# Kernel optimization log

Hardware: AMD Instinct MI355X
Metric: run time of the kernel (lower is better)

Reference implementation:

```python
import jax, jax.numpy as jnp
import numpy as np

SCALE = 0.2  # init_kwargs: scale
EPS = 1e-12  # F.normalize default eps


def setup_inputs() -> dict:
    key = jax.random.key(0)
    x = jax.random.normal(key, (8, 2048, 512), dtype=jnp.float32)
    return {"x": x}


def reference(x):
    # x: [B, N, D]
    # F.normalize(x, dim=2): x / max(||x||_2, eps)
    norm = jnp.linalg.norm(x, axis=2, keepdims=True)
    x_norm = x / jnp.maximum(norm, EPS)
    # sim: [B, N, N] = x_norm @ x_norm^T, softmax over last dim
    sim = jnp.einsum('bnd,bmd->bnm', x_norm, x_norm)
    attn = jax.nn.softmax(sim, axis=2)
    # (1 + scale) * x - scale * attn @ x
    out = (1.0 + SCALE) * x - SCALE * jnp.einsum('bnm,bmd->bnd', attn, x)
    return out
```

## Files before the change

kernel.cpp:

```cpp
#include <hip/hip_runtime.h>
#include <stdint.h>

typedef unsigned short ushort_t;
typedef float f32x2 __attribute__((ext_vector_type(2)));
typedef float f32x4 __attribute__((ext_vector_type(4)));
typedef float f32x16 __attribute__((ext_vector_type(16)));
typedef short bf16x8 __attribute__((ext_vector_type(8)));
typedef unsigned short us8 __attribute__((ext_vector_type(8)));

#define BATCH 8
#define SEQ   2048
#define DIM   512
#define KBLK  64
#define NIT   (SEQ / KBLK)
#define LDS_TOTAL 156160

__device__ __forceinline__ ushort_t f2bf(float f) {
  union { float f; uint32_t u; } c; c.f = f;
  uint32_t u = c.u;
  return (ushort_t)((u + 0x7FFFu + ((u >> 16) & 1u)) >> 16);
}
__device__ __forceinline__ uint32_t packbf(float a, float b) {
  return (uint32_t)f2bf(a) | ((uint32_t)f2bf(b) << 16);
}
__device__ __forceinline__ void gload_lds16(const void* g, void* l) {
  __builtin_amdgcn_global_load_lds(
      (const __attribute__((address_space(1))) unsigned int*)g,
      (__attribute__((address_space(3))) unsigned int*)l, 16, 0, 0);
}
#define WAIT_LGKM_BAR() { asm volatile("s_waitcnt lgkmcnt(0)" ::: "memory"); \
  __builtin_amdgcn_s_barrier(); __builtin_amdgcn_sched_barrier(0); }
#define WAIT_ALL_BAR()  { asm volatile("s_waitcnt vmcnt(0) lgkmcnt(0)" ::: "memory"); \
  __builtin_amdgcn_s_barrier(); __builtin_amdgcn_sched_barrier(0); }

__global__ void k_prep(const float* __restrict__ x, ushort_t* __restrict__ xn,
                       ushort_t* __restrict__ vt) {
  __shared__ __align__(16) ushort_t tile[64][512];
  const int tid = threadIdx.x, lane = tid & 63, w = tid >> 6;
  const int b = blockIdx.x >> 5, nt = blockIdx.x & 31;
  const size_t row0 = (size_t)b * SEQ + (size_t)nt * 64;

  for (int j = 0; j < 16; ++j) {
    const int r = w * 16 + j;
    const float* xr = x + (row0 + r) * DIM;
    const float4 a  = ((const float4*)xr)[lane * 2];
    const float4 bb = ((const float4*)xr)[lane * 2 + 1];
    float ss = a.x*a.x + a.y*a.y + a.z*a.z + a.w*a.w
             + bb.x*bb.x + bb.y*bb.y + bb.z*bb.z + bb.w*bb.w;
#pragma unroll
    for (int m = 32; m >= 1; m >>= 1) ss += __shfl_xor(ss, m, 64);
    const float rn = 1.2011224087864498f / sqrtf(fmaxf(ss, 1e-24f));
    us8 nrm, raw;
    nrm[0]=f2bf(a.x*rn);  nrm[1]=f2bf(a.y*rn);  nrm[2]=f2bf(a.z*rn);  nrm[3]=f2bf(a.w*rn);
    nrm[4]=f2bf(bb.x*rn); nrm[5]=f2bf(bb.y*rn); nrm[6]=f2bf(bb.z*rn); nrm[7]=f2bf(bb.w*rn);
    raw[0]=f2bf(a.x);  raw[1]=f2bf(a.y);  raw[2]=f2bf(a.z);  raw[3]=f2bf(a.w);
    raw[4]=f2bf(bb.x); raw[5]=f2bf(bb.y); raw[6]=f2bf(bb.z); raw[7]=f2bf(bb.w);
    *(us8*)(xn + (row0 + r) * DIM + lane * 8) = nrm;
    *(us8*)(&tile[r][lane * 8]) = raw;
  }
  __syncthreads();
#pragma unroll
  for (int pass = 0; pass < 2; ++pass) {
    const int d = pass * 256 + tid;
    ushort_t* dst = vt + ((size_t)b * DIM + d) * SEQ + (size_t)nt * 64;
#pragma unroll
    for (int g = 0; g < 8; ++g) {
      us8 v;
#pragma unroll
      for (int e = 0; e < 8; ++e) v[e] = tile[g * 8 + e][d];
      *(us8*)(dst + g * 8) = v;
    }
  }
}

__launch_bounds__(512, 2)
__global__ void k_attn(const ushort_t* __restrict__ xn, const ushort_t* __restrict__ vt,
                       const float* __restrict__ x, float* __restrict__ out) {
  extern __shared__ char smem[];
  char* const Kb0 = smem;
  char* const Kb1 = smem + 65536;
  ushort_t* const P = (ushort_t*)(smem + 131072);
  float* const Sp   = (float*)(smem + 139264);
  float* const lsum = (float*)(smem + 155648);

  const int tid = threadIdx.x;
  const int lane = tid & 63, w = tid >> 6;
  const int kw = w & 1, qw = (w >> 1) & 1, kd = w >> 2;
  const int l31 = lane & 31, l5 = lane >> 5, l7 = lane & 7;
  const int b = blockIdx.x & 7, qt0 = blockIdx.x >> 3;
  const int q0 = qt0 * 64;

  const ushort_t* xnb = xn + (size_t)b * SEQ * DIM;
  const ushort_t* vtb = vt + (size_t)b * DIM * SEQ;

  bf16x8 qreg[16];
#pragma unroll
  for (int ks = 0; ks < 16; ++ks)
    qreg[ks] = *(const bf16x8*)(xnb + (size_t)(q0 + qw * 32 + l31) * DIM
                                + kd * 256 + ks * 16 + l5 * 8);

  f32x16 acc[2][2] = {};
  float plsum = 0.f;

#pragma unroll
  for (int i = 0; i < 8; ++i) {
    const int row = w * 8 + i;
    gload_lds16(xnb + (size_t)row * DIM + ((lane ^ i) << 3), Kb0 + row * 1024);
  }
  asm volatile("s_waitcnt vmcnt(0)" ::: "memory");
  __builtin_amdgcn_s_barrier();
  __builtin_amdgcn_sched_barrier(0);

  for (int t = 0; t < NIT; ++t) {
    const int k0 = t * KBLK;
    char* const Kc = (t & 1) ? Kb1 : Kb0;
    char* const Kn = (t & 1) ? Kb0 : Kb1;

    f32x16 accS = {};
    const int arow = kw * 32 + l31;
#pragma unroll
    for (int ks = 0; ks < 16; ++ks) {
      const int c = kd * 32 + ks * 2 + l5;
      bf16x8 af = *(const bf16x8*)(Kc + arow * 1024 + ((c ^ l7) << 4));
      accS = __builtin_amdgcn_mfma_f32_32x32x16_bf16(af, qreg[ks], accS, 0, 0, 0);
    }

    if (kd) {
      float* tile = Sp + (kw * 2 + qw) * 1024 + l31 * 32;
#pragma unroll
      for (int j = 0; j < 8; ++j) {
        const int u = (j & 1) + 4 * (j >> 1) + 2 * l5;
        f32x2 v = { accS[2 * j], accS[2 * j + 1] };
        *(f32x2*)(tile + ((u ^ l7) << 1)) = v;
      }
    }
    WAIT_LGKM_BAR();

    bf16x8 vv[2][4];
#pragma unroll
    for (int dt = 0; dt < 2; ++dt)
#pragma unroll
      for (int ks = 0; ks < 4; ++ks)
        vv[dt][ks] = *(const bf16x8*)(vtb + (size_t)(w * 64 + dt * 32 + l31) * SEQ
                                      + k0 + ks * 16 + l5 * 8);

    if (!kd) {
      const float* tile = Sp + (kw * 2 + qw) * 1024 + l31 * 32;
      uint32_t* prow = (uint32_t*)(P + (qw * 32 + l31) * 64);
#pragma unroll
      for (int j = 0; j < 8; ++j) {
        const int u = (j & 1) + 4 * (j >> 1) + 2 * l5;
        f32x2 o = *(const f32x2*)(tile + ((u ^ l7) << 1));
        float p0 = __builtin_amdgcn_exp2f(accS[2 * j]     + o[0]);
        float p1 = __builtin_amdgcn_exp2f(accS[2 * j + 1] + o[1]);
        plsum += p0 + p1;
        const int chunk = (kw * 4 + (j >> 1)) ^ l7;
        prow[chunk * 4 + (j & 1) + 2 * l5] = packbf(p0, p1);
      }
    } else if (t + 1 < NIT) {
      const int sid = w - 4;
#pragma unroll
      for (int i = 0; i < 16; ++i) {
        const int row = sid * 16 + i;
        gload_lds16(xnb + (size_t)(k0 + KBLK + row) * DIM + ((lane ^ (i & 7)) << 3),
                    Kn + row * 1024);
      }
    }
    WAIT_LGKM_BAR();

#pragma unroll
    for (int qt = 0; qt < 2; ++qt) {
#pragma unroll
      for (int ks = 0; ks < 4; ++ks) {
        const int c = (ks * 2 + l5) ^ l7;
        bf16x8 pa = *(const bf16x8*)(P + (qt * 32 + l31) * 64 + c * 8);
        acc[qt][0] = __builtin_amdgcn_mfma_f32_32x32x16_bf16(pa, vv[0][ks], acc[qt][0], 0, 0, 0);
        acc[qt][1] = __builtin_amdgcn_mfma_f32_32x32x16_bf16(pa, vv[1][ks], acc[qt][1], 0, 0, 0);
      }
    }
    WAIT_ALL_BAR();
  }

  if (!kd) {
    plsum += __shfl_xor(plsum, 32, 64);
    if (lane < 32) lsum[kw * 64 + qw * 32 + lane] = plsum;
  }
  float* obuf = (float*)smem;
#pragma unroll
  for (int qt = 0; qt < 2; ++qt)
#pragma unroll
    for (int dt = 0; dt < 2; ++dt) {
      const int d = w * 64 + dt * 32 + l31;
#pragma unroll
      for (int r = 0; r < 16; ++r) {
        const int q = qt * 32 + (r & 3) + 8 * (r >> 2) + 4 * l5;
        const int c = (d >> 2) ^ (q & 7);
        obuf[q * 512 + c * 4 + (d & 3)] = acc[qt][dt][r];
      }
    }
  WAIT_LGKM_BAR();

  const int q = tid >> 3, seg = tid & 7;
  const float s = 0.2f / (lsum[q] + lsum[64 + q]);
  const size_t grow = ((size_t)b * SEQ + q0 + q) * DIM;
#pragma unroll
  for (int i = 0; i < 16; ++i) {
    const int c = seg * 16 + i;
    const int cs = c ^ (q & 7);
    f32x4 a = *(const f32x4*)(obuf + q * 512 + cs * 4);
    const float4 xv = *(const float4*)(x + grow + c * 4);
    float4 o;
    o.x = 1.2f * xv.x - s * a[0];
    o.y = 1.2f * xv.y - s * a[1];
    o.z = 1.2f * xv.z - s * a[2];
    o.w = 1.2f * xv.w - s * a[3];
    *(float4*)(out + grow + c * 4) = o;
  }
}

extern "C" void kernel_launch(void* const* d_in, const int* in_sizes, int n_in,
                              void* d_out, int out_size, void* d_ws, size_t ws_size,
                              hipStream_t stream) {
  const float* x = (const float*)d_in[0];
  float* out = (float*)d_out;
  ushort_t* xn = (ushort_t*)d_ws;
  ushort_t* vt = (ushort_t*)((char*)d_ws + (size_t)BATCH * SEQ * DIM * 2);

  k_prep<<<BATCH * (SEQ / 64), 256, 0, stream>>>(x, xn, vt);
  (void)hipFuncSetAttribute((const void*)k_attn,
                            hipFuncAttributeMaxDynamicSharedMemorySize, LDS_TOTAL);
  k_attn<<<BATCH * SEQ / 64, 512, LDS_TOTAL, stream>>>(xn, vt, x, out);
}
```

Baseline: 226.4 us.

## Rewrite attention with warp-specialized QK/PV waves and fragment-major K/V layouts

Replaces both kernels. The prep kernel now writes normalized K and raw V in MFMA-fragment-major tiled layouts. In the attention kernel, Q is staged once in LDS, and four waves compute QK^T while loading the next K fragments straight into registers. The other four waves do the exp, the P write and the PV MFMAs one step behind, using double-buffered P. This aims to overlap the two matmul phases across waves, remove the LDS double buffer for K, and reduce LDS use. The cost is a serialized two-barrier handoff per tile, heavy register pressure, and an uncoalesced scalar output epilogue.

```diff
diff --git a/kernel.cpp b/kernel.cpp
--- a/kernel.cpp
+++ b/kernel.cpp
@@ -11,211 +11,250 @@
 #define BATCH 8
 #define SEQ   2048
 #define DIM   512
-#define KBLK  64
-#define NIT   (SEQ / KBLK)
-#define LDS_TOTAL 156160
+#define NIT   32
 
 __device__ __forceinline__ ushort_t f2bf(float f) {
   union { float f; uint32_t u; } c; c.f = f;
-  uint32_t u = c.u;
-  return (ushort_t)((u + 0x7FFFu + ((u >> 16) & 1u)) >> 16);
-}
-__device__ __forceinline__ uint32_t packbf(float a, float b) {
-  return (uint32_t)f2bf(a) | ((uint32_t)f2bf(b) << 16);
-}
-__device__ __forceinline__ void gload_lds16(const void* g, void* l) {
-  __builtin_amdgcn_global_load_lds(
-      (const __attribute__((address_space(1))) unsigned int*)g,
-      (__attribute__((address_space(3))) unsigned int*)l, 16, 0, 0);
-}
-#define WAIT_LGKM_BAR() { asm volatile("s_waitcnt lgkmcnt(0)" ::: "memory"); \
-  __builtin_amdgcn_s_barrier(); __builtin_amdgcn_sched_barrier(0); }
-#define WAIT_ALL_BAR()  { asm volatile("s_waitcnt vmcnt(0) lgkmcnt(0)" ::: "memory"); \
-  __builtin_amdgcn_s_barrier(); __builtin_amdgcn_sched_barrier(0); }
-
-__global__ void k_prep(const float* __restrict__ x, ushort_t* __restrict__ xn,
-                       ushort_t* __restrict__ vt) {
-  __shared__ __align__(16) ushort_t tile[64][512];
+  return (ushort_t)((c.u + 0x7FFFu + ((c.u >> 16) & 1u)) >> 16);
+}
+
+__global__ __launch_bounds__(256) void k_prep(const float* __restrict__ x,
+                                              ushort_t* __restrict__ kg,
+                                              ushort_t* __restrict__ vg) {
+  __shared__ ushort_t ln[32 * 512];
+  __shared__ ushort_t rw[32 * 512];
   const int tid = threadIdx.x, lane = tid & 63, w = tid >> 6;
-  const int b = blockIdx.x >> 5, nt = blockIdx.x & 31;
-  const size_t row0 = (size_t)b * SEQ + (size_t)nt * 64;
-
-  for (int j = 0; j < 16; ++j) {
-    const int r = w * 16 + j;
-    const float* xr = x + (row0 + r) * DIM;
-    const float4 a  = ((const float4*)xr)[lane * 2];
-    const float4 bb = ((const float4*)xr)[lane * 2 + 1];
+  const int bs = blockIdx.x;
+  const int b = bs >> 6, sib = bs & 63;
+  const float* xs = x + (size_t)bs * 32 * DIM;
+  ushort_t* kgs = kg + (size_t)bs * 32 * DIM;
+  ushort_t* vgb = vg + (size_t)b * SEQ * DIM;
+
+#pragma unroll
+  for (int j = 0; j < 8; ++j) {
+    const int rl = w * 8 + j;
+    const float4 a = *(const float4*)(xs + (size_t)rl * DIM + lane * 8);
+    const float4 c = *(const float4*)(xs + (size_t)rl * DIM + lane * 8 + 4);
     float ss = a.x*a.x + a.y*a.y + a.z*a.z + a.w*a.w
-             + bb.x*bb.x + bb.y*bb.y + bb.z*bb.z + bb.w*bb.w;
+             + c.x*c.x + c.y*c.y + c.z*c.z + c.w*c.w;
 #pragma unroll
     for (int m = 32; m >= 1; m >>= 1) ss += __shfl_xor(ss, m, 64);
     const float rn = 1.2011224087864498f / sqrtf(fmaxf(ss, 1e-24f));
-    us8 nrm, raw;
-    nrm[0]=f2bf(a.x*rn);  nrm[1]=f2bf(a.y*rn);  nrm[2]=f2bf(a.z*rn);  nrm[3]=f2bf(a.w*rn);
-    nrm[4]=f2bf(bb.x*rn); nrm[5]=f2bf(bb.y*rn); nrm[6]=f2bf(bb.z*rn); nrm[7]=f2bf(bb.w*rn);
-    raw[0]=f2bf(a.x);  raw[1]=f2bf(a.y);  raw[2]=f2bf(a.z);  raw[3]=f2bf(a.w);
-    raw[4]=f2bf(bb.x); raw[5]=f2bf(bb.y); raw[6]=f2bf(bb.z); raw[7]=f2bf(bb.w);
-    *(us8*)(xn + (row0 + r) * DIM + lane * 8) = nrm;
-    *(us8*)(&tile[r][lane * 8]) = raw;
+    us8 nv, rv;
+    nv[0]=f2bf(a.x*rn); nv[1]=f2bf(a.y*rn); nv[2]=f2bf(a.z*rn); nv[3]=f2bf(a.w*rn);
+    nv[4]=f2bf(c.x*rn); nv[5]=f2bf(c.y*rn); nv[6]=f2bf(c.z*rn); nv[7]=f2bf(c.w*rn);
+    rv[0]=f2bf(a.x); rv[1]=f2bf(a.y); rv[2]=f2bf(a.z); rv[3]=f2bf(a.w);
+    rv[4]=f2bf(c.x); rv[5]=f2bf(c.y); rv[6]=f2bf(c.z); rv[7]=f2bf(c.w);
+    *(us8*)(&ln[rl * 512 + ((lane ^ rl) << 3)]) = nv;
+    *(us8*)(&rw[rl * 512 + ((lane ^ rl) << 3)]) = rv;
   }
   __syncthreads();
-#pragma unroll
-  for (int pass = 0; pass < 2; ++pass) {
-    const int d = pass * 256 + tid;
-    ushort_t* dst = vt + ((size_t)b * DIM + d) * SEQ + (size_t)nt * 64;
-#pragma unroll
-    for (int g = 0; g < 8; ++g) {
-      us8 v;
-#pragma unroll
-      for (int e = 0; e < 8; ++e) v[e] = tile[g * 8 + e][d];
-      *(us8*)(dst + g * 8) = v;
-    }
-  }
-}
-
-__launch_bounds__(512, 2)
-__global__ void k_attn(const ushort_t* __restrict__ xn, const ushort_t* __restrict__ vt,
-                       const float* __restrict__ x, float* __restrict__ out) {
+
+  const int k32 = tid & 31, g = tid >> 5;
+#pragma unroll
+  for (int p = 0; p < 4; ++p) {
+    const int ks = p * 8 + g;
+    const us8 e0 = *(const us8*)(&ln[k32 * 512 + (((2 * ks)     ^ k32) << 3)]);
+    const us8 e1 = *(const us8*)(&ln[k32 * 512 + (((2 * ks + 1) ^ k32) << 3)]);
+    *(us8*)(kgs + ks * 512 + k32 * 16)     = e0;
+    *(us8*)(kgs + ks * 512 + k32 * 16 + 8) = e1;
+  }
+#pragma unroll
+  for (int p = 0; p < 4; ++p) {
+    const int blk = p * 8 + g;
+    const int kh = blk >> 4, db = blk & 15;
+    const int cch = db * 4 + (k32 >> 3);
+    us8 v0, v1;
+#pragma unroll
+    for (int j = 0; j < 8; ++j) {
+      const int ka = kh * 16 + j;
+      const int kb = kh * 16 + 8 + j;
+      v0[j] = rw[ka * 512 + ((cch ^ ka) << 3) + (k32 & 7)];
+      v1[j] = rw[kb * 512 + ((cch ^ kb) << 3) + (k32 & 7)];
+    }
+    ushort_t* dst = vgb + ((size_t)(sib * 2 + kh) * 16 + db) * 512 + k32 * 16;
+    *(us8*)(dst)     = v0;
+    *(us8*)(dst + 8) = v1;
+  }
+}
+
+#define LSP   65536
+#define LP0   98304
+#define LP1   106496
+#define LRED  114688
+#define LDS_TOTAL 115712
+
+__global__ __launch_bounds__(512, 2) void k_attn(const ushort_t* __restrict__ kg,
+                                                 const ushort_t* __restrict__ vg,
+                                                 const float* __restrict__ x,
+                                                 float* __restrict__ out) {
   extern __shared__ char smem[];
-  char* const Kb0 = smem;
-  char* const Kb1 = smem + 65536;
-  ushort_t* const P = (ushort_t*)(smem + 131072);
-  float* const Sp   = (float*)(smem + 139264);
-  float* const lsum = (float*)(smem + 155648);
-
-  const int tid = threadIdx.x;
-  const int lane = tid & 63, w = tid >> 6;
-  const int kw = w & 1, qw = (w >> 1) & 1, kd = w >> 2;
-  const int l31 = lane & 31, l5 = lane >> 5, l7 = lane & 7;
+  ushort_t* const Qs = (ushort_t*)smem;
+  float* const Sp = (float*)(smem + LSP);
+  float* const lred = (float*)(smem + LRED);
+
+  const int tid = threadIdx.x, lane = tid & 63, w = tid >> 6;
+  const int l31 = lane & 31, l5 = lane >> 5;
   const int b = blockIdx.x & 7, qt0 = blockIdx.x >> 3;
-  const int q0 = qt0 * 64;
-
-  const ushort_t* xnb = xn + (size_t)b * SEQ * DIM;
-  const ushort_t* vtb = vt + (size_t)b * DIM * SEQ;
-
-  bf16x8 qreg[16];
-#pragma unroll
-  for (int ks = 0; ks < 16; ++ks)
-    qreg[ks] = *(const bf16x8*)(xnb + (size_t)(q0 + qw * 32 + l31) * DIM
-                                + kd * 256 + ks * 16 + l5 * 8);
-
-  f32x16 acc[2][2] = {};
+  const ushort_t* kgb = kg + (size_t)b * SEQ * DIM;
+  const ushort_t* vgb = vg + (size_t)b * SEQ * DIM;
+
+  {
+    const int r = tid >> 3;
+    const size_t strip = (size_t)(qt0 * 2 + (r >> 5));
+#pragma unroll
+    for (int it = 0; it < 8; ++it) {
+      const int s = it * 8 + (tid & 7);
+      const int c = s ^ (r & 31);
+      const bf16x8 v = *(const bf16x8*)(kgb + strip * 16384
+                          + (c >> 1) * 512 + (r & 31) * 16 + (c & 1) * 8);
+      *(bf16x8*)(Qs + r * 512 + s * 8) = v;
+    }
+  }
+  const bool isQK = (w < 4);
+  const int kw = w & 1, kd = (w >> 1) & 1;
+  const int jv = w - 4;
+
+  bf16x8 acur[16];
+  bf16x8 vcur[16];
+  f32x16 acc[2][4];
   float plsum = 0.f;
 
-#pragma unroll
-  for (int i = 0; i < 8; ++i) {
-    const int row = w * 8 + i;
-    gload_lds16(xnb + (size_t)row * DIM + ((lane ^ i) << 3), Kb0 + row * 1024);
-  }
-  asm volatile("s_waitcnt vmcnt(0)" ::: "memory");
+  if (isQK) {
+#pragma unroll
+    for (int ks = 0; ks < 16; ++ks)
+      acur[ks] = *(const bf16x8*)(kgb + (size_t)kw * 16384
+                    + (kd * 16 + ks) * 512 + l31 * 16 + l5 * 8);
+  } else {
+    const f32x16 z = {};
+#pragma unroll
+    for (int qt = 0; qt < 2; ++qt)
+#pragma unroll
+      for (int dt = 0; dt < 4; ++dt) acc[qt][dt] = z;
+  }
+  asm volatile("s_waitcnt lgkmcnt(0)" ::: "memory");
   __builtin_amdgcn_s_barrier();
   __builtin_amdgcn_sched_barrier(0);
 
   for (int t = 0; t < NIT; ++t) {
-    const int k0 = t * KBLK;
-    char* const Kc = (t & 1) ? Kb1 : Kb0;
-    char* const Kn = (t & 1) ? Kb0 : Kb1;
-
-    f32x16 accS = {};
-    const int arow = kw * 32 + l31;
-#pragma unroll
-    for (int ks = 0; ks < 16; ++ks) {
-      const int c = kd * 32 + ks * 2 + l5;
-      bf16x8 af = *(const bf16x8*)(Kc + arow * 1024 + ((c ^ l7) << 4));
-      accS = __builtin_amdgcn_mfma_f32_32x32x16_bf16(af, qreg[ks], accS, 0, 0, 0);
-    }
-
-    if (kd) {
-      float* tile = Sp + (kw * 2 + qw) * 1024 + l31 * 32;
-#pragma unroll
-      for (int j = 0; j < 8; ++j) {
-        const int u = (j & 1) + 4 * (j >> 1) + 2 * l5;
-        f32x2 v = { accS[2 * j], accS[2 * j + 1] };
-        *(f32x2*)(tile + ((u ^ l7) << 1)) = v;
-      }
-    }
-    WAIT_LGKM_BAR();
-
-    bf16x8 vv[2][4];
-#pragma unroll
-    for (int dt = 0; dt < 2; ++dt)
-#pragma unroll
-      for (int ks = 0; ks < 4; ++ks)
-        vv[dt][ks] = *(const bf16x8*)(vtb + (size_t)(w * 64 + dt * 32 + l31) * SEQ
-                                      + k0 + ks * 16 + l5 * 8);
-
-    if (!kd) {
-      const float* tile = Sp + (kw * 2 + qw) * 1024 + l31 * 32;
-      uint32_t* prow = (uint32_t*)(P + (qw * 32 + l31) * 64);
-#pragma unroll
-      for (int j = 0; j < 8; ++j) {
-        const int u = (j & 1) + 4 * (j >> 1) + 2 * l5;
-        f32x2 o = *(const f32x2*)(tile + ((u ^ l7) << 1));
-        float p0 = __builtin_amdgcn_exp2f(accS[2 * j]     + o[0]);
-        float p1 = __builtin_amdgcn_exp2f(accS[2 * j + 1] + o[1]);
-        plsum += p0 + p1;
-        const int chunk = (kw * 4 + (j >> 1)) ^ l7;
-        prow[chunk * 4 + (j & 1) + 2 * l5] = packbf(p0, p1);
-      }
-    } else if (t + 1 < NIT) {
-      const int sid = w - 4;
-#pragma unroll
-      for (int i = 0; i < 16; ++i) {
-        const int row = sid * 16 + i;
-        gload_lds16(xnb + (size_t)(k0 + KBLK + row) * DIM + ((lane ^ (i & 7)) << 3),
-                    Kn + row * 1024);
-      }
-    }
-    WAIT_LGKM_BAR();
-
-#pragma unroll
-    for (int qt = 0; qt < 2; ++qt) {
+    char* const Pprev = smem + ((t & 1) ? LP0 : LP1);
+    char* const Pcur  = smem + ((t & 1) ? LP1 : LP0);
+
+    if (isQK) {
+      const int tn = (t + 1 < NIT) ? (t + 1) : t;
+      const ushort_t* abase = kgb + (size_t)(2 * tn + kw) * 16384;
+      f32x16 s0 = {}, s1 = {};
+#pragma unroll
+      for (int ks = 0; ks < 16; ++ks) {
+        const int cc = kd * 32 + ks * 2 + l5;
+        const bf16x8 b0 = *(const bf16x8*)(Qs + l31 * 512 + ((cc ^ l31) << 3));
+        const bf16x8 b1 = *(const bf16x8*)(Qs + (32 + l31) * 512 + ((cc ^ l31) << 3));
+        s0 = __builtin_amdgcn_mfma_f32_32x32x16_bf16(acur[ks], b0, s0, 0, 0, 0);
+        s1 = __builtin_amdgcn_mfma_f32_32x32x16_bf16(acur[ks], b1, s1, 0, 0, 0);
+        acur[ks] = *(const bf16x8*)(abase + (kd * 16 + ks) * 512 + l31 * 16 + l5 * 8);
+      }
+      float* const sw = Sp + (kw * 2 + kd) * 2048;
+#pragma unroll
+      for (int qt = 0; qt < 2; ++qt) {
+        const int q = qt * 32 + l31;
+        const f32x16 sv = qt ? s1 : s0;
+#pragma unroll
+        for (int mm = 0; mm < 4; ++mm) {
+          const int u0 = 4 * mm + 2 * l5;
+          const f32x2 p0 = { sv[4 * mm],     sv[4 * mm + 1] };
+          const f32x2 p1 = { sv[4 * mm + 2], sv[4 * mm + 3] };
+          *(f32x2*)(sw + q * 32 + ((u0 ^ (l31 & 15)) << 1))       = p0;
+          *(f32x2*)(sw + q * 32 + (((u0 + 1) ^ (l31 & 15)) << 1)) = p1;
+        }
+      }
+      asm volatile("s_waitcnt lgkmcnt(0)" ::: "memory");
+      __builtin_amdgcn_sched_barrier(0);
+    } else {
+      if (t > 0) {
+#pragma unroll
+        for (int qt = 0; qt < 2; ++qt)
+#pragma unroll
+          for (int ks = 0; ks < 4; ++ks) {
+            const bf16x8 pa = *(const bf16x8*)(Pprev + (qt * 32 + l31) * 128
+                                + (((ks * 2 + l5) ^ (l31 & 7)) << 4));
+#pragma unroll
+            for (int dt = 0; dt < 4; ++dt)
+              acc[qt][dt] = __builtin_amdgcn_mfma_f32_32x32x16_bf16(
+                  pa, vcur[dt * 4 + ks], acc[qt][dt], 0, 0, 0);
+          }
+      }
+#pragma unroll
+      for (int dt = 0; dt < 4; ++dt)
+#pragma unroll
+        for (int ks = 0; ks < 4; ++ks)
+          vcur[dt * 4 + ks] = *(const bf16x8*)(vgb
+              + ((size_t)(t * 4 + ks) * 16 + jv * 4 + dt) * 512 + l31 * 16 + l5 * 8);
+    }
+    __builtin_amdgcn_s_barrier();
+    __builtin_amdgcn_sched_barrier(0);
+
+    if (!isQK) {
+      const float* sr0 = Sp + ((jv >> 1) * 2 + 0) * 2048 + lane * 32;
+      const float* sr1 = Sp + ((jv >> 1) * 2 + 1) * 2048 + lane * 32;
+      float pv[16];
+#pragma unroll
+      for (int m2 = 0; m2 < 8; ++m2) {
+        const int u = (((jv & 1) * 8 + m2) ^ (lane & 15)) << 1;
+        const f32x2 a0 = *(const f32x2*)(sr0 + u);
+        const f32x2 a1 = *(const f32x2*)(sr1 + u);
+        pv[2 * m2]     = __builtin_amdgcn_exp2f(a0[0] + a1[0]);
+        pv[2 * m2 + 1] = __builtin_amdgcn_exp2f(a0[1] + a1[1]);
+      }
+      us8 w0, w1;
+#pragma unroll
+      for (int m = 0; m < 8; ++m) {
+        w0[m] = f2bf(pv[m]); w1[m] = f2bf(pv[8 + m]);
+        plsum += pv[m] + pv[8 + m];
+      }
+      *(us8*)(Pcur + lane * 128 + (((jv * 2)     ^ (lane & 7)) << 4)) = w0;
+      *(us8*)(Pcur + lane * 128 + (((jv * 2 + 1) ^ (lane & 7)) << 4)) = w1;
+      asm volatile("s_waitcnt lgkmcnt(0)" ::: "memory");
+      __builtin_amdgcn_sched_barrier(0);
+    }
+    __builtin_amdgcn_s_barrier();
+    __builtin_amdgcn_sched_barrier(0);
+  }
+
+  if (!isQK) {
+    char* const Pl = smem + LP1;
+#pragma unroll
+    for (int qt = 0; qt < 2; ++qt)
 #pragma unroll
       for (int ks = 0; ks < 4; ++ks) {
-        const int c = (ks * 2 + l5) ^ l7;
-        bf16x8 pa = *(const bf16x8*)(P + (qt * 32 + l31) * 64 + c * 8);
-        acc[qt][0] = __builtin_amdgcn_mfma_f32_32x32x16_bf16(pa, vv[0][ks], acc[qt][0], 0, 0, 0);
-        acc[qt][1] = __builtin_amdgcn_mfma_f32_32x32x16_bf16(pa, vv[1][ks], acc[qt][1], 0, 0, 0);
-      }
-    }
-    WAIT_ALL_BAR();
-  }
-
-  if (!kd) {
-    plsum += __shfl_xor(plsum, 32, 64);
-    if (lane < 32) lsum[kw * 64 + qw * 32 + lane] = plsum;
-  }
-  float* obuf = (float*)smem;
+        const bf16x8 pa = *(const bf16x8*)(Pl + (qt * 32 + l31) * 128
+                            + (((ks * 2 + l5) ^ (l31 & 7)) << 4));
+#pragma unroll
+        for (int dt = 0; dt < 4; ++dt)
+          acc[qt][dt] = __builtin_amdgcn_mfma_f32_32x32x16_bf16(
+              pa, vcur[dt * 4 + ks], acc[qt][dt], 0, 0, 0);
+      }
+    lred[jv * 64 + lane] = plsum;
+    asm volatile("s_waitcnt lgkmcnt(0)" ::: "memory");
+  }
+  __builtin_amdgcn_s_barrier();
+  __builtin_amdgcn_sched_barrier(0);
+  if (isQK) return;
+
+  const size_t rowb = (size_t)b * SEQ + qt0 * 64;
 #pragma unroll
   for (int qt = 0; qt < 2; ++qt)
 #pragma unroll
-    for (int dt = 0; dt < 2; ++dt) {
-      const int d = w * 64 + dt * 32 + l31;
-#pragma unroll
-      for (int r = 0; r < 16; ++r) {
-        const int q = qt * 32 + (r & 3) + 8 * (r >> 2) + 4 * l5;
-        const int c = (d >> 2) ^ (q & 7);
-        obuf[q * 512 + c * 4 + (d & 3)] = acc[qt][dt][r];
-      }
-    }
-  WAIT_LGKM_BAR();
-
-  const int q = tid >> 3, seg = tid & 7;
-  const float s = 0.2f / (lsum[q] + lsum[64 + q]);
-  const size_t grow = ((size_t)b * SEQ + q0 + q) * DIM;
-#pragma unroll
-  for (int i = 0; i < 16; ++i) {
-    const int c = seg * 16 + i;
-    const int cs = c ^ (q & 7);
-    f32x4 a = *(const f32x4*)(obuf + q * 512 + cs * 4);
-    const float4 xv = *(const float4*)(x + grow + c * 4);
-    float4 o;
-    o.x = 1.2f * xv.x - s * a[0];
-    o.y = 1.2f * xv.y - s * a[1];
-    o.z = 1.2f * xv.z - s * a[2];
-    o.w = 1.2f * xv.w - s * a[3];
-    *(float4*)(out + grow + c * 4) = o;
-  }
+    for (int r = 0; r < 16; ++r) {
+      const int q = qt * 32 + (r & 3) + 8 * (r >> 2) + 4 * l5;
+      const float lq = lred[q] + lred[64 + q] + lred[128 + q] + lred[192 + q];
+      const float sc = 0.2f / lq;
+#pragma unroll
+      for (int dt = 0; dt < 4; ++dt) {
+        const int d = jv * 128 + dt * 32 + l31;
+        const size_t gi = (rowb + q) * DIM + d;
+        out[gi] = 1.2f * x[gi] - sc * acc[qt][dt][r];
+      }
+    }
 }
 
 extern "C" void kernel_launch(void* const* d_in, const int* in_sizes, int n_in,
@@ -223,11 +262,11 @@
                               hipStream_t stream) {
   const float* x = (const float*)d_in[0];
   float* out = (float*)d_out;
-  ushort_t* xn = (ushort_t*)d_ws;
-  ushort_t* vt = (ushort_t*)((char*)d_ws + (size_t)BATCH * SEQ * DIM * 2);
-
-  k_prep<<<BATCH * (SEQ / 64), 256, 0, stream>>>(x, xn, vt);
+  ushort_t* kg = (ushort_t*)d_ws;
+  ushort_t* vg = (ushort_t*)((char*)d_ws + (size_t)BATCH * SEQ * DIM * 2);
+
+  k_prep<<<BATCH * SEQ / 32, 256, 0, stream>>>(x, kg, vg);
   (void)hipFuncSetAttribute((const void*)k_attn,
                             hipFuncAttributeMaxDynamicSharedMemorySize, LDS_TOTAL);
-  k_attn<<<BATCH * SEQ / 64, 512, LDS_TOTAL, stream>>>(xn, vt, x, out);
-}
+  k_attn<<<BATCH * SEQ / 64, 512, LDS_TOTAL, stream>>>(kg, vg, x, out);
+}
```

Result: slower. 510.4 us (+125.5%).
